# Kernel optimization log

Hardware: AMD Instinct MI355X
Metric: run time of the kernel (lower is better)

## Reference

```python
import math
import jax, jax.numpy as jnp
import numpy as np

B, S, DIM = 2, 2048, 512
H = 8
HD = DIM // H          # 64
WIN = 64               # window_size (even)


def setup_inputs() -> dict:
    key = jax.random.key(0)
    kx, kq, ko = jax.random.split(key, 3)
    x = jax.random.normal(kx, (B, S, DIM), jnp.float32)
    # torch Linear(dim, 3*dim, bias=False): y = x @ W^T; we store the transposed weight directly
    Wqkv = jax.random.normal(kq, (DIM, 3 * DIM), jnp.float32) / math.sqrt(DIM)
    Wout = jax.random.normal(ko, (DIM, DIM), jnp.float32) / math.sqrt(DIM)
    return {"x": x, "Wqkv": Wqkv, "Wout": Wout}


def reference(x, Wqkv, Wout):
    b, s, d = x.shape
    half = WIN // 2
    # qkv projection -> (3, B, H, S, HD)
    qkv = (x @ Wqkv).reshape(b, s, 3, H, HD).transpose(2, 0, 3, 1, 4)
    q, k, v = qkv[0], qkv[1], qkv[2]
    # zero-pad along sequence: half on left, half-1 on right (matches F.pad + unfold)
    k_pad = jnp.pad(k, ((0, 0), (0, 0), (half, half - 1), (0, 0)))
    v_pad = jnp.pad(v, ((0, 0), (0, 0), (half, half - 1), (0, 0)))
    idx = jnp.arange(s)[:, None] + jnp.arange(WIN)[None, :]
    k_win = k_pad[:, :, idx]
    v_win = v_pad[:, :, idx]
    scores = jnp.einsum('bhid,bhiwd->bhiw', q, k_win) / math.sqrt(HD)
    # NOTE: no masking of zero-padded slots, faithful to the torch baseline
    attn = jax.nn.softmax(scores, axis=-1)
    out = jnp.einsum('bhiw,bhiwd->bhid', attn, v_win)
    out = out.transpose(0, 2, 1, 3).reshape(b, s, d)
    return out @ Wout
```

## Files before the change

kernel.cpp:

```cpp
#include <hip/hip_runtime.h>


#define S_SZ   2048
#define DIMM   512
#define NH     8
#define HDIM   64
#define MROWS  4096
#define NQKV   1536

typedef _Float16 half8 __attribute__((ext_vector_type(8)));
typedef _Float16 half4 __attribute__((ext_vector_type(4)));
typedef float    f32x4 __attribute__((ext_vector_type(4)));

#define GLOAD16(g, l)                                                          \
  __builtin_amdgcn_global_load_lds(                                            \
      (const __attribute__((address_space(1))) void*)(g),                      \
      (__attribute__((address_space(3))) void*)(l), 16, 0, 0)

__global__ __launch_bounds__(256) void prep_fused(const float* __restrict__ x,
                                                  const float* __restrict__ Wqkv,
                                                  const float* __restrict__ Wout,
                                                  _Float16* __restrict__ xb,
                                                  _Float16* __restrict__ WqkvT,
                                                  _Float16* __restrict__ WoutT) {
  __shared__ float tile[32][33];
  const int blk = blockIdx.x;
  if (blk < 2048) {
    int i = (blk * 256 + threadIdx.x) * 4;
    float4 v = *reinterpret_cast<const float4*>(x + i);
    half4 h;
    h[0] = (_Float16)v.x; h[1] = (_Float16)v.y; h[2] = (_Float16)v.z; h[3] = (_Float16)v.w;
    *reinterpret_cast<half4*>(xb + i) = h;
    return;
  }
  const float* in;  _Float16* out;  int K, N, bx, by;
  if (blk < 2816) { in = Wqkv; out = WqkvT; K = 512; N = 1536; int r = blk - 2048; bx = r % 48; by = r / 48; }
  else            { in = Wout; out = WoutT; K = 512; N = 512;  int r = blk - 2816; bx = r % 16; by = r / 16; }
  const int n0 = bx * 32, k0 = by * 32;
  const int tx = threadIdx.x & 31, ty = threadIdx.x >> 5;
#pragma unroll
  for (int i = 0; i < 4; i++) {
    int k = ty + i * 8;
    tile[k][tx] = in[(size_t)(k0 + k) * N + n0 + tx];
  }
  __syncthreads();
#pragma unroll
  for (int i = 0; i < 4; i++) {
    int n = ty + i * 8;
    out[(size_t)(n0 + n) * K + k0 + tx] = (_Float16)tile[tx][n];
  }
}

template <bool C_F16>
__global__ __launch_bounds__(256) void gemm_f16(const _Float16* __restrict__ A,
                                                const _Float16* __restrict__ BT,
                                                void* __restrict__ C,
                                                int M, int N, int K) {
  __shared__ _Float16 As[128 * 32];
  __shared__ _Float16 Bs[128 * 32];

  const int brow = blockIdx.y * 128, bcol = blockIdx.x * 128;
  const int tid = threadIdx.x;
  const int lane = tid & 63, wid = tid >> 6;
  const int wm = (wid >> 1) * 64, wn = (wid & 1) * 64;

  f32x4 acc[4][4] = {};

  const int srow = wid * 32 + (lane >> 2);
  const int scol = (lane & 3) * 8;
  _Float16* lA = As + wid * 1024;
  _Float16* lB = Bs + wid * 1024;

  const int fr = lane & 15, kb = (lane >> 4) * 8;

  for (int kt = 0; kt < K; kt += 32) {
    const _Float16* ga = A  + (size_t)(brow + srow) * K + kt + scol;
    const _Float16* gb = BT + (size_t)(bcol + srow) * K + kt + scol;
    GLOAD16(ga, lA);
    GLOAD16(ga + (size_t)16 * K, lA + 512);
    GLOAD16(gb, lB);
    GLOAD16(gb + (size_t)16 * K, lB + 512);
    __syncthreads();

    half8 af[4], bf[4];
#pragma unroll
    for (int m = 0; m < 4; m++) af[m] = *(const half8*)(As + (wm + m * 16 + fr) * 32 + kb);
#pragma unroll
    for (int n = 0; n < 4; n++) bf[n] = *(const half8*)(Bs + (wn + n * 16 + fr) * 32 + kb);
#pragma unroll
    for (int m = 0; m < 4; m++)
#pragma unroll
      for (int n = 0; n < 4; n++)
        acc[m][n] = __builtin_amdgcn_mfma_f32_16x16x32_f16(af[m], bf[n], acc[m][n], 0, 0, 0);
    __syncthreads();
  }

  const int fq = lane >> 4;
#pragma unroll
  for (int m = 0; m < 4; m++)
#pragma unroll
    for (int n = 0; n < 4; n++)
#pragma unroll
      for (int j = 0; j < 4; j++) {
        int rr = brow + wm + m * 16 + fq * 4 + j;
        int cc = bcol + wn + n * 16 + fr;
        if (C_F16) ((_Float16*)C)[(size_t)rr * N + cc] = (_Float16)acc[m][n][j];
        else       ((float*)C)[(size_t)rr * N + cc]    = acc[m][n][j];
      }
}

__device__ __forceinline__ int swz(int row, int colh) {
  int key = ((row & 7) ^ ((row >> 3) & 7)) << 4;
  return row * 128 + (((colh * 2) ^ key) >> 1);
}

__global__ __launch_bounds__(256) void attn_mfma(const _Float16* __restrict__ qkv,
                                                 _Float16* __restrict__ attn_out) {
  __shared__ _Float16 Vt[64 * 128];
  __shared__ _Float16 Pl[64 * 128];

  const int b = blockIdx.z, h = blockIdx.y, q0 = blockIdx.x * 64;
  const int kv0 = q0 - 32;
  const int tid = threadIdx.x;
  const int lane = tid & 63, w = tid >> 6;
  const int fr = lane & 15, g = lane >> 4;

  {
    const int jg = tid >> 3, dg = tid & 7;
    half8 vv[4];
#pragma unroll
    for (int i = 0; i < 4; i++) {
      int s = kv0 + jg * 4 + i;
      half8 z = {};
      if (s >= 0 && s < S_SZ)
        z = *(const half8*)(qkv + (size_t)(b * S_SZ + s) * NQKV + 2 * DIMM + h * HDIM + dg * 8);
      vv[i] = z;
    }
#pragma unroll
    for (int i2 = 0; i2 < 8; i2++) {
      half4 o;
      o[0] = vv[0][i2]; o[1] = vv[1][i2]; o[2] = vv[2][i2]; o[3] = vv[3][i2];
      *(half4*)(Vt + swz(dg * 8 + i2, jg * 4)) = o;
    }
  }

  const _Float16* qbase = qkv + (size_t)(b * S_SZ + q0 + 16 * w + fr) * NQKV + h * HDIM;
  half8 bq0 = *(const half8*)(qbase + 8 * g);
  half8 bq1 = *(const half8*)(qbase + 32 + 8 * g);

  f32x4 st[8];
#pragma unroll
  for (int kt = 0; kt < 8; kt++) st[kt] = (f32x4){0.f, 0.f, 0.f, 0.f};

#pragma unroll
  for (int kt = 0; kt < 8; kt++) {
    int s = kv0 + 16 * kt + fr;
    half8 a0 = {}, a1 = {};
    if (s >= 0 && s < S_SZ) {
      const _Float16* kb2 = qkv + (size_t)(b * S_SZ + s) * NQKV + DIMM + h * HDIM;
      a0 = *(const half8*)(kb2 + 8 * g);
      a1 = *(const half8*)(kb2 + 32 + 8 * g);
    }
    st[kt] = __builtin_amdgcn_mfma_f32_16x16x32_f16(a0, bq0, st[kt], 0, 0, 0);
    st[kt] = __builtin_amdgcn_mfma_f32_16x16x32_f16(a1, bq1, st[kt], 0, 0, 0);
  }

  const int qi = 16 * w + fr;
  float m = -1e30f;
#pragma unroll
  for (int kt = 0; kt < 8; kt++)
#pragma unroll
    for (int j = 0; j < 4; j++) {
      int krel = 16 * kt + 4 * g + j;
      float scv = st[kt][j] * 0.125f;
      st[kt][j] = scv;
      if (krel >= qi && krel < qi + 64) m = fmaxf(m, scv);
    }
  m = fmaxf(m, __shfl_xor(m, 16));
  m = fmaxf(m, __shfl_xor(m, 32));
  float sum = 0.f;
#pragma unroll
  for (int kt = 0; kt < 8; kt++)
#pragma unroll
    for (int j = 0; j < 4; j++) {
      int krel = 16 * kt + 4 * g + j;
      float p = (krel >= qi && krel < qi + 64) ? __expf(st[kt][j] - m) : 0.f;
      st[kt][j] = p;
      sum += p;
    }
  sum += __shfl_xor(sum, 16);
  sum += __shfl_xor(sum, 32);
  const float inv = 1.f / sum;
#pragma unroll
  for (int kt = 0; kt < 8; kt++) {
    half4 o;
#pragma unroll
    for (int j = 0; j < 4; j++) o[j] = (_Float16)(st[kt][j] * inv);
    *(half4*)(Pl + swz(qi, 16 * kt + 4 * g)) = o;
  }

  __syncthreads();

  f32x4 acc[4];
#pragma unroll
  for (int dt = 0; dt < 4; dt++) acc[dt] = (f32x4){0.f, 0.f, 0.f, 0.f};
  half8 ap[4];
#pragma unroll
  for (int ks = 0; ks < 4; ks++)
    ap[ks] = *(const half8*)(Pl + swz(16 * w + fr, 32 * ks + 8 * g));
#pragma unroll
  for (int dt = 0; dt < 4; dt++)
#pragma unroll
    for (int ks = 0; ks < 4; ks++) {
      half8 bv = *(const half8*)(Vt + swz(16 * dt + fr, 32 * ks + 8 * g));
      acc[dt] = __builtin_amdgcn_mfma_f32_16x16x32_f16(ap[ks], bv, acc[dt], 0, 0, 0);
    }

#pragma unroll
  for (int dt = 0; dt < 4; dt++)
#pragma unroll
    for (int j = 0; j < 4; j++) {
      int q = q0 + 16 * w + 4 * g + j;
      attn_out[(size_t)(b * S_SZ + q) * DIMM + h * HDIM + 16 * dt + fr] = (_Float16)acc[dt][j];
    }
}

extern "C" void kernel_launch(void* const* d_in, const int* in_sizes, int n_in,
                              void* d_out, int out_size, void* d_ws, size_t ws_size,
                              hipStream_t stream) {
  const float* x    = (const float*)d_in[0];
  const float* Wqkv = (const float*)d_in[1];
  const float* Wout = (const float*)d_in[2];

  char* ws = (char*)d_ws;
  _Float16* xb    = (_Float16*)(ws);
  _Float16* WqkvT = (_Float16*)(ws + 4194304);
  _Float16* WoutT = (_Float16*)(ws + 5767168);
  _Float16* qkv   = (_Float16*)(ws + 6291456);
  _Float16* attn  = (_Float16*)(ws + 18874368);

  prep_fused<<<3072, 256, 0, stream>>>(x, Wqkv, Wout, xb, WqkvT, WoutT);
  gemm_f16<true><<<dim3(12, 32), 256, 0, stream>>>(xb, WqkvT, (void*)qkv, MROWS, NQKV, DIMM);
  attn_mfma<<<dim3(32, NH, 2), 256, 0, stream>>>(qkv, attn);
  gemm_f16<false><<<dim3(4, 32), 256, 0, stream>>>(attn, WoutT, d_out, MROWS, DIMM, DIMM);
}
```

Baseline: 107.6 us.

## Double-buffer GEMM LDS tiles and stage attention keys through shared memory

The GEMM kernel gets two LDS buffers per operand, so the async global-to-LDS load of the next K-tile is issued before the MFMA work on the current tile. The aim is to overlap global memory latency with compute, at the cost of twice the shared memory per block. The attention kernel now loads the 128-key window cooperatively into an XOR-swizzled LDS buffer once per block. Before, each of the four waves read the same keys from global memory on its own. The barrier before the P·V stage moves up to sit after the K and V staging, since each wave only reads back the P rows it wrote itself.

Result: faster. 103.4 us (-3.9%).

```diff
diff --git a/kernel.cpp b/kernel.cpp
--- a/kernel.cpp
+++ b/kernel.cpp
@@ -56,8 +56,8 @@
                                                 const _Float16* __restrict__ BT,
                                                 void* __restrict__ C,
                                                 int M, int N, int K) {
-  __shared__ _Float16 As[128 * 32];
-  __shared__ _Float16 Bs[128 * 32];
+  __shared__ _Float16 As[2][128 * 32];
+  __shared__ _Float16 Bs[2][128 * 32];
 
   const int brow = blockIdx.y * 128, bcol = blockIdx.x * 128;
   const int tid = threadIdx.x;
@@ -68,32 +68,46 @@
 
   const int srow = wid * 32 + (lane >> 2);
   const int scol = (lane & 3) * 8;
-  _Float16* lA = As + wid * 1024;
-  _Float16* lB = Bs + wid * 1024;
-
   const int fr = lane & 15, kb = (lane >> 4) * 8;
 
-  for (int kt = 0; kt < K; kt += 32) {
-    const _Float16* ga = A  + (size_t)(brow + srow) * K + kt + scol;
-    const _Float16* gb = BT + (size_t)(bcol + srow) * K + kt + scol;
-    GLOAD16(ga, lA);
-    GLOAD16(ga + (size_t)16 * K, lA + 512);
-    GLOAD16(gb, lB);
-    GLOAD16(gb + (size_t)16 * K, lB + 512);
-    __syncthreads();
+  const _Float16* gaBase = A  + (size_t)(brow + srow) * K + scol;
+  const _Float16* gbBase = BT + (size_t)(bcol + srow) * K + scol;
+
+#define STAGE(buf, kt)                                                         \
+  do {                                                                         \
+    const _Float16* ga = gaBase + (kt);                                        \
+    const _Float16* gb = gbBase + (kt);                                        \
+    _Float16* lA = As[buf] + wid * 1024;                                       \
+    _Float16* lB = Bs[buf] + wid * 1024;                                       \
+    GLOAD16(ga, lA);                                                           \
+    GLOAD16(ga + (size_t)16 * K, lA + 512);                                    \
+    GLOAD16(gb, lB);                                                           \
+    GLOAD16(gb + (size_t)16 * K, lB + 512);                                    \
+  } while (0)
+
+  STAGE(0, 0);
+  __syncthreads();
+
+  const int NT = K >> 5;
+  int cur = 0;
+  for (int t = 0; t < NT; t++) {
+    if (t + 1 < NT) STAGE(cur ^ 1, (t + 1) * 32);
 
     half8 af[4], bf[4];
 #pragma unroll
-    for (int m = 0; m < 4; m++) af[m] = *(const half8*)(As + (wm + m * 16 + fr) * 32 + kb);
-#pragma unroll
-    for (int n = 0; n < 4; n++) bf[n] = *(const half8*)(Bs + (wn + n * 16 + fr) * 32 + kb);
+    for (int m = 0; m < 4; m++) af[m] = *(const half8*)(As[cur] + (wm + m * 16 + fr) * 32 + kb);
+#pragma unroll
+    for (int n = 0; n < 4; n++) bf[n] = *(const half8*)(Bs[cur] + (wn + n * 16 + fr) * 32 + kb);
 #pragma unroll
     for (int m = 0; m < 4; m++)
 #pragma unroll
       for (int n = 0; n < 4; n++)
         acc[m][n] = __builtin_amdgcn_mfma_f32_16x16x32_f16(af[m], bf[n], acc[m][n], 0, 0, 0);
+
     __syncthreads();
-  }
+    cur ^= 1;
+  }
+#undef STAGE
 
   const int fq = lane >> 4;
 #pragma unroll
@@ -118,6 +132,7 @@
                                                  _Float16* __restrict__ attn_out) {
   __shared__ _Float16 Vt[64 * 128];
   __shared__ _Float16 Pl[64 * 128];
+  __shared__ _Float16 Ks[128 * 64];
 
   const int b = blockIdx.z, h = blockIdx.y, q0 = blockIdx.x * 64;
   const int kv0 = q0 - 32;
@@ -142,25 +157,34 @@
       o[0] = vv[0][i2]; o[1] = vv[1][i2]; o[2] = vv[2][i2]; o[3] = vv[3][i2];
       *(half4*)(Vt + swz(dg * 8 + i2, jg * 4)) = o;
     }
+    const int k0r = tid >> 3;
+#pragma unroll
+    for (int i = 0; i < 4; i++) {
+      int key = k0r + i * 32;
+      int s = kv0 + key;
+      half8 z = {};
+      if (s >= 0 && s < S_SZ)
+        z = *(const half8*)(qkv + (size_t)(b * S_SZ + s) * NQKV + DIMM + h * HDIM + dg * 8);
+      int slot = dg ^ (key & 7);
+      *(half8*)(Ks + key * 64 + slot * 8) = z;
+    }
   }
 
   const _Float16* qbase = qkv + (size_t)(b * S_SZ + q0 + 16 * w + fr) * NQKV + h * HDIM;
   half8 bq0 = *(const half8*)(qbase + 8 * g);
   half8 bq1 = *(const half8*)(qbase + 32 + 8 * g);
 
+  __syncthreads();
+
   f32x4 st[8];
 #pragma unroll
   for (int kt = 0; kt < 8; kt++) st[kt] = (f32x4){0.f, 0.f, 0.f, 0.f};
-
 #pragma unroll
   for (int kt = 0; kt < 8; kt++) {
-    int s = kv0 + 16 * kt + fr;
-    half8 a0 = {}, a1 = {};
-    if (s >= 0 && s < S_SZ) {
-      const _Float16* kb2 = qkv + (size_t)(b * S_SZ + s) * NQKV + DIMM + h * HDIM;
-      a0 = *(const half8*)(kb2 + 8 * g);
-      a1 = *(const half8*)(kb2 + 32 + 8 * g);
-    }
+    const int key = 16 * kt + fr;
+    const int s0 = g ^ (key & 7), s1 = (g + 4) ^ (key & 7);
+    half8 a0 = *(const half8*)(Ks + key * 64 + s0 * 8);
+    half8 a1 = *(const half8*)(Ks + key * 64 + s1 * 8);
     st[kt] = __builtin_amdgcn_mfma_f32_16x16x32_f16(a0, bq0, st[kt], 0, 0, 0);
     st[kt] = __builtin_amdgcn_mfma_f32_16x16x32_f16(a1, bq1, st[kt], 0, 0, 0);
   }
@@ -198,8 +222,6 @@
     for (int j = 0; j < 4; j++) o[j] = (_Float16)(st[kt][j] * inv);
     *(half4*)(Pl + swz(qi, 16 * kt + 4 * g)) = o;
   }
-
-  __syncthreads();
 
   f32x4 acc[4];
 #pragma unroll
```
